# Performance work log

Measured on AMD Instinct MI355X. Metric: run time of the kernel, lower is better.

The kernel has to match this reference:

```python
import jax, jax.numpy as jnp
import numpy as np

N_CELL = 50000
N_GENE = 50000
E = 800000
D = 256
EPS = 1e-5


def setup_inputs() -> dict:
    key = jax.random.key(0)
    ks = jax.random.split(key, 12)
    inp = {
        "x_cell": jax.random.normal(ks[0], (N_CELL, D), jnp.float32),
        "x_gene": jax.random.normal(ks[1], (N_GENE, D), jnp.float32),
        "W_cg": jax.random.normal(ks[2], (D, D), jnp.float32) * (1.0 / np.sqrt(D)),
        "W_gc": jax.random.normal(ks[3], (D, D), jnp.float32) * (1.0 / np.sqrt(D)),
        "W_gg": jax.random.normal(ks[4], (D, D), jnp.float32) * (1.0 / np.sqrt(D)),
        "gamma_cell": jnp.ones((D,), jnp.float32),
        "beta_cell": jnp.zeros((D,), jnp.float32),
        "gamma_gene": jnp.ones((D,), jnp.float32),
        "beta_gene": jnp.zeros((D,), jnp.float32),
        "b_cell": jnp.zeros((D,), jnp.float32),
        "b_gene": jnp.zeros((D,), jnp.float32),
        "src_cg": jax.random.randint(ks[5], (E,), 0, N_CELL, jnp.int64 if jax.config.jax_enable_x64 else jnp.int32),
        "dst_cg": jax.random.randint(ks[6], (E,), 0, N_GENE, jnp.int64 if jax.config.jax_enable_x64 else jnp.int32),
        "src_gc": jax.random.randint(ks[7], (E,), 0, N_GENE, jnp.int64 if jax.config.jax_enable_x64 else jnp.int32),
        "dst_gc": jax.random.randint(ks[8], (E,), 0, N_CELL, jnp.int64 if jax.config.jax_enable_x64 else jnp.int32),
        "src_gg": jax.random.randint(ks[9], (E,), 0, N_GENE, jnp.int64 if jax.config.jax_enable_x64 else jnp.int32),
        "dst_gg": jax.random.randint(ks[10], (E,), 0, N_GENE, jnp.int64 if jax.config.jax_enable_x64 else jnp.int32),
    }
    return inp


def _graph_conv(x_src, src, dst, n_src, n_dst, W):
    """DGL GraphConv with norm='both': D_dst^{-1/2} A D_src^{-1/2} X W."""
    ones = jnp.ones(src.shape[0], x_src.dtype)
    deg_out = jnp.clip(jax.ops.segment_sum(ones, src, num_segments=n_src), 1.0)
    deg_in = jnp.clip(jax.ops.segment_sum(ones, dst, num_segments=n_dst), 1.0)
    h = x_src * jax.lax.rsqrt(deg_out)[:, None]          # [n_src, D]
    agg = jax.ops.segment_sum(h[src], dst, num_segments=n_dst)  # gather+scatter
    agg = agg * jax.lax.rsqrt(deg_in)[:, None]           # [n_dst, D]
    return agg @ W


def _post(h, gamma, beta, b):
    # LayerNorm (affine) -> + h_bias -> relu -> dropout(p=0, eval = identity)
    mu = jnp.mean(h, axis=-1, keepdims=True)
    var = jnp.mean((h - mu) ** 2, axis=-1, keepdims=True)
    h = (h - mu) * jax.lax.rsqrt(var + EPS) * gamma + beta
    return jax.nn.relu(h + b)


def reference(x_cell, x_gene, W_cg, W_gc, W_gg, gamma_cell, beta_cell,
              gamma_gene, beta_gene, b_cell, b_gene,
              src_cg, dst_cg, src_gc, dst_gc, src_gg, dst_gg):
    # HeteroGraphConv with aggregate='sum' across relations per dst ntype
    h_gene = (_graph_conv(x_cell, src_cg, dst_cg, N_CELL, N_GENE, W_cg)
              + _graph_conv(x_gene, src_gg, dst_gg, N_GENE, N_GENE, W_gg))
    h_cell = _graph_conv(x_gene, src_gc, dst_gc, N_GENE, N_CELL, W_gc)
    out_cell = _post(h_cell, gamma_cell, beta_cell, b_cell)
    out_gene = _post(h_gene, gamma_gene, beta_gene, b_gene)
    return jnp.stack([out_cell, out_gene])  # [2, 50000, 256]
```

## Files before the change

kernel.cpp:

```cpp
#include <hip/hip_runtime.h>
#include <hip/hip_bf16.h>
#include <stdint.h>

#define DDIM 256
#define NSHARD 8
#define T1 4096
#define NCPAD 128
#define CCAP 9216

typedef short s8v __attribute__((ext_vector_type(8)));
typedef float f4v __attribute__((ext_vector_type(4)));

__device__ __forceinline__ float bf2f(unsigned u) { return __uint_as_float(u << 16); }
__device__ __forceinline__ unsigned short f2bf(float f) {
    __hip_bfloat16 h = __float2bfloat16(f);
    return *reinterpret_cast<unsigned short*>(&h);
}
__device__ __forceinline__ unsigned pack2(float a, float b) {
    return (unsigned)f2bf(a) | ((unsigned)f2bf(b) << 16);
}

__global__ void transpose3_k(const float* __restrict__ W0, const float* __restrict__ W1,
                             const float* __restrict__ W2, __hip_bfloat16* __restrict__ T0,
                             __hip_bfloat16* __restrict__ T1v, __hip_bfloat16* __restrict__ T2) {
    const float* W = (blockIdx.y == 0) ? W0 : (blockIdx.y == 1) ? W1 : W2;
    __hip_bfloat16* T = (blockIdx.y == 0) ? T0 : (blockIdx.y == 1) ? T1v : T2;
    T[blockIdx.x * DDIM + threadIdx.x] = __float2bfloat16(W[threadIdx.x * DDIM + blockIdx.x]);
}

__global__ __launch_bounds__(256) void bin1_k(
    const int* __restrict__ s0, const int* __restrict__ d0,
    const int* __restrict__ s1, const int* __restrict__ d1,
    const int* __restrict__ s2, const int* __restrict__ d2,
    int* __restrict__ cs_shard,
    int* __restrict__ gcur,
    unsigned* __restrict__ recs,
    int N, int E) {
    __shared__ unsigned stage[T1];
    __shared__ int hcnt[NCPAD], hoff[NCPAD], lbase[NCPAD], lcur[NCPAD];
    const int t = threadIdx.x;
    const int rel = blockIdx.y;
    const int* s = (rel == 0) ? s0 : (rel == 1) ? s1 : s2;
    const int* d = (rel == 0) ? d0 : (rel == 1) ? d1 : d2;
    const int e0 = blockIdx.x * T1;
    const int n = min(T1, E - e0);
    int* csb = cs_shard + ((size_t)(blockIdx.x & (NSHARD - 1)) * 3 + rel) * N;

    if (t < NCPAD) { hcnt[t] = 0; lcur[t] = 0; }
    __syncthreads();

    int ssr[T1 / 256], ddr[T1 / 256];
    #pragma unroll
    for (int k = 0; k < T1 / 256; ++k) {
        const int li = k * 256 + t;
        const bool v = li < n;
        ssr[k] = v ? s[e0 + li] : -1;
        ddr[k] = v ? d[e0 + li] : -1;
        if (v) {
            atomicAdd(&hcnt[ddr[k] >> 9], 1);
            atomicAdd(&csb[ssr[k]], 1);
        }
    }
    __syncthreads();

    if (t < 64) {
        const int a0 = hcnt[2 * t], a1 = hcnt[2 * t + 1];
        const int sum = a0 + a1;
        int incl = sum;
        #pragma unroll
        for (int off = 1; off < 64; off <<= 1) {
            const int u = __shfl_up(incl, off);
            if (t >= off) incl += u;
        }
        const int excl = incl - sum;
        hoff[2 * t] = excl;
        hoff[2 * t + 1] = excl + a0;
    }
    __syncthreads();
    if (t < NCPAD) lbase[t] = atomicAdd(&gcur[rel * NCPAD + t], hcnt[t]);
    __syncthreads();

    #pragma unroll
    for (int k = 0; k < T1 / 256; ++k) {
        if (ddr[k] >= 0) {
            const int b = ddr[k] >> 9;
            const int p = atomicAdd(&lcur[b], 1);
            stage[hoff[b] + p] = (unsigned)ssr[k] | ((unsigned)(ddr[k] & 511) << 16)
                                 | ((unsigned)b << 25);
        }
    }
    __syncthreads();

    for (int i = t; i < n; i += 256) {
        const unsigned r = stage[i];
        const int b = (int)(r >> 25);
        const int pos = lbase[b] + (i - hoff[b]);
        if (pos < CCAP)
            recs[((size_t)rel * NCPAD + b) * CCAP + pos] = r & 0x1FFFFFFu;
    }
}

__global__ void reduce_cs_k(const int* __restrict__ cs_shard, int* __restrict__ cs, int n3) {
    const int i = blockIdx.x * blockDim.x + threadIdx.x;
    if (i >= n3) return;
    int v = 0;
    #pragma unroll
    for (int s = 0; s < NSHARD; ++s) v += cs_shard[(size_t)s * n3 + i];
    cs[i] = v;
}

__global__ __launch_bounds__(256) void sort_k(
    unsigned* __restrict__ recs, const int* __restrict__ gcur,
    int* __restrict__ row_beg, int* __restrict__ row_cnt, int N, int ncb) {
    __shared__ unsigned stage[CCAP];
    __shared__ int rc[512], ro[512], rcur[512];
    const int t = threadIdx.x;
    const int rel = blockIdx.x / ncb, bin = blockIdx.x % ncb;
    const size_t base = ((size_t)rel * NCPAD + bin) * CCAP;
    const int n = min(gcur[rel * NCPAD + bin], CCAP);

    for (int i = t; i < 512; i += 256) rc[i] = 0;
    __syncthreads();
    for (int i = t; i < n; i += 256) {
        const unsigned r = recs[base + i];
        stage[i] = r;
        atomicAdd(&rc[(r >> 16) & 511], 1);
    }
    __syncthreads();
    if (t < 64) {
        int v[8], p[8], sum = 0;
        #pragma unroll
        for (int j = 0; j < 8; ++j) { v[j] = rc[t * 8 + j]; p[j] = sum; sum += v[j]; }
        int incl = sum;
        #pragma unroll
        for (int off = 1; off < 64; off <<= 1) {
            const int u = __shfl_up(incl, off);
            if (t >= off) incl += u;
        }
        const int excl = incl - sum;
        #pragma unroll
        for (int j = 0; j < 8; ++j) { ro[t * 8 + j] = excl + p[j]; rcur[t * 8 + j] = excl + p[j]; }
    }
    __syncthreads();
    for (int i = t; i < 512; i += 256) {
        const int grow = bin * 512 + i;
        if (grow < N) {
            row_cnt[(size_t)rel * N + grow] = rc[i];
            row_beg[(size_t)rel * N + grow] = (int)(base + ro[i]);
        }
    }
    for (int i = t; i < n; i += 256) {
        const unsigned r = stage[i];
        const int pos = atomicAdd(&rcur[(r >> 16) & 511], 1);
        recs[base + pos] = r & 0xffffu;
    }
}

__global__ __launch_bounds__(256, 2) void gemm2_k(
    const float* __restrict__ X,
    const __hip_bfloat16* __restrict__ Wt0, const __hip_bfloat16* __restrict__ Wt1,
    const int* __restrict__ deg0, const int* __restrict__ deg1,
    __hip_bfloat16* __restrict__ Y0, __hip_bfloat16* __restrict__ Y1, int M) {
    const int lane = threadIdx.x & 63, wid = threadIdx.x >> 6;
    const int c = lane & 15, kb = lane >> 4;
    const int rA = blockIdx.x * 128 + wid * 32 + c;
    const int rB = rA + 16;
    const bool vA = rA < M, vB = rB < M;
    const int rAc = vA ? rA : (M - 1), rBc = vB ? rB : (M - 1);

    s8v xfA[8], xfB[8];
    const float* xA = X + (size_t)rAc * DDIM;
    const float* xB = X + (size_t)rBc * DDIM;
    #pragma unroll
    for (int ks = 0; ks < 8; ++ks) {
        const int k0 = ks * 32 + kb * 8;
        const f4v a0 = *reinterpret_cast<const f4v*>(xA + k0);
        const f4v a1 = *reinterpret_cast<const f4v*>(xA + k0 + 4);
        const f4v b0 = *reinterpret_cast<const f4v*>(xB + k0);
        const f4v b1 = *reinterpret_cast<const f4v*>(xB + k0 + 4);
        union { s8v v; unsigned short u[8]; } fa, fb;
        #pragma unroll
        for (int j = 0; j < 4; ++j) {
            fa.u[j] = f2bf(a0[j]); fa.u[4 + j] = f2bf(a1[j]);
            fb.u[j] = f2bf(b0[j]); fb.u[4 + j] = f2bf(b1[j]);
        }
        xfA[ks] = fa.v; xfB[ks] = fb.v;
    }

    const int dA0 = deg0[rAc], dB0 = deg0[rBc], dA1 = deg1[rAc], dB1 = deg1[rBc];
    const float s0A = rsqrtf((float)(dA0 < 1 ? 1 : dA0));
    const float s0B = rsqrtf((float)(dB0 < 1 ? 1 : dB0));
    const float s1A = rsqrtf((float)(dA1 < 1 ? 1 : dA1));
    const float s1B = rsqrtf((float)(dB1 < 1 ? 1 : dB1));

    #pragma unroll 2
    for (int nt = 0; nt < 16; ++nt) {
        const __hip_bfloat16* w0p = Wt0 + (size_t)(nt * 16 + c) * DDIM + kb * 8;
        const __hip_bfloat16* w1p = Wt1 + (size_t)(nt * 16 + c) * DDIM + kb * 8;
        s8v wf0[8], wf1[8];
        #pragma unroll
        for (int ks = 0; ks < 8; ++ks) {
            wf0[ks] = *reinterpret_cast<const s8v*>(w0p + ks * 32);
            wf1[ks] = *reinterpret_cast<const s8v*>(w1p + ks * 32);
        }
        f4v a00 = (f4v){0.f,0.f,0.f,0.f}, a01 = a00, a10 = a00, a11 = a00;
        #pragma unroll
        for (int ks = 0; ks < 8; ++ks) {
            a00 = __builtin_amdgcn_mfma_f32_16x16x32_bf16(wf0[ks], xfA[ks], a00, 0, 0, 0);
            a10 = __builtin_amdgcn_mfma_f32_16x16x32_bf16(wf0[ks], xfB[ks], a10, 0, 0, 0);
            a01 = __builtin_amdgcn_mfma_f32_16x16x32_bf16(wf1[ks], xfA[ks], a01, 0, 0, 0);
            a11 = __builtin_amdgcn_mfma_f32_16x16x32_bf16(wf1[ks], xfB[ks], a11, 0, 0, 0);
        }
        const int col = nt * 16 + kb * 4;
        if (vA) {
            uint2 o0, o1;
            o0.x = pack2(a00[0] * s0A, a00[1] * s0A); o0.y = pack2(a00[2] * s0A, a00[3] * s0A);
            o1.x = pack2(a01[0] * s1A, a01[1] * s1A); o1.y = pack2(a01[2] * s1A, a01[3] * s1A);
            *reinterpret_cast<uint2*>(Y0 + (size_t)rA * DDIM + col) = o0;
            *reinterpret_cast<uint2*>(Y1 + (size_t)rA * DDIM + col) = o1;
        }
        if (vB) {
            uint2 o0, o1;
            o0.x = pack2(a10[0] * s0B, a10[1] * s0B); o0.y = pack2(a10[2] * s0B, a10[3] * s0B);
            o1.x = pack2(a11[0] * s1B, a11[1] * s1B); o1.y = pack2(a11[2] * s1B, a11[3] * s1B);
            *reinterpret_cast<uint2*>(Y0 + (size_t)rB * DDIM + col) = o0;
            *reinterpret_cast<uint2*>(Y1 + (size_t)rB * DDIM + col) = o1;
        }
    }
}

__global__ __launch_bounds__(256, 2) void gemm1_k(
    const float* __restrict__ X, const __hip_bfloat16* __restrict__ Wt0,
    const int* __restrict__ deg0, __hip_bfloat16* __restrict__ Y0, int M) {
    const int lane = threadIdx.x & 63, wid = threadIdx.x >> 6;
    const int c = lane & 15, kb = lane >> 4;
    const int rA = blockIdx.x * 128 + wid * 32 + c;
    const int rB = rA + 16;
    const bool vA = rA < M, vB = rB < M;
    const int rAc = vA ? rA : (M - 1), rBc = vB ? rB : (M - 1);

    s8v xfA[8], xfB[8];
    const float* xA = X + (size_t)rAc * DDIM;
    const float* xB = X + (size_t)rBc * DDIM;
    #pragma unroll
    for (int ks = 0; ks < 8; ++ks) {
        const int k0 = ks * 32 + kb * 8;
        const f4v a0 = *reinterpret_cast<const f4v*>(xA + k0);
        const f4v a1 = *reinterpret_cast<const f4v*>(xA + k0 + 4);
        const f4v b0 = *reinterpret_cast<const f4v*>(xB + k0);
        const f4v b1 = *reinterpret_cast<const f4v*>(xB + k0 + 4);
        union { s8v v; unsigned short u[8]; } fa, fb;
        #pragma unroll
        for (int j = 0; j < 4; ++j) {
            fa.u[j] = f2bf(a0[j]); fa.u[4 + j] = f2bf(a1[j]);
            fb.u[j] = f2bf(b0[j]); fb.u[4 + j] = f2bf(b1[j]);
        }
        xfA[ks] = fa.v; xfB[ks] = fb.v;
    }
    const int dA0 = deg0[rAc], dB0 = deg0[rBc];
    const float s0A = rsqrtf((float)(dA0 < 1 ? 1 : dA0));
    const float s0B = rsqrtf((float)(dB0 < 1 ? 1 : dB0));

    #pragma unroll 2
    for (int nt = 0; nt < 16; ++nt) {
        const __hip_bfloat16* w0p = Wt0 + (size_t)(nt * 16 + c) * DDIM + kb * 8;
        s8v wf0[8];
        #pragma unroll
        for (int ks = 0; ks < 8; ++ks) wf0[ks] = *reinterpret_cast<const s8v*>(w0p + ks * 32);
        f4v a00 = (f4v){0.f,0.f,0.f,0.f}, a10 = a00;
        #pragma unroll
        for (int ks = 0; ks < 8; ++ks) {
            a00 = __builtin_amdgcn_mfma_f32_16x16x32_bf16(wf0[ks], xfA[ks], a00, 0, 0, 0);
            a10 = __builtin_amdgcn_mfma_f32_16x16x32_bf16(wf0[ks], xfB[ks], a10, 0, 0, 0);
        }
        const int col = nt * 16 + kb * 4;
        if (vA) {
            uint2 o;
            o.x = pack2(a00[0] * s0A, a00[1] * s0A); o.y = pack2(a00[2] * s0A, a00[3] * s0A);
            *reinterpret_cast<uint2*>(Y0 + (size_t)rA * DDIM + col) = o;
        }
        if (vB) {
            uint2 o;
            o.x = pack2(a10[0] * s0B, a10[1] * s0B); o.y = pack2(a10[2] * s0B, a10[3] * s0B);
            *reinterpret_cast<uint2*>(Y0 + (size_t)rB * DDIM + col) = o;
        }
    }
}

__device__ __forceinline__ void addv(f4v& a, uint2 v) {
    a[0] += bf2f(v.x & 0xffffu);
    a[1] += bf2f(v.x >> 16);
    a[2] += bf2f(v.y & 0xffffu);
    a[3] += bf2f(v.y >> 16);
}

__device__ __forceinline__ f4v segsum(const unsigned* __restrict__ recs, int beg, int n,
                                      const __hip_bfloat16* __restrict__ Y, int lane) {
    f4v a = (f4v){0.f, 0.f, 0.f, 0.f};
    for (int j0 = 0; j0 < n; j0 += 64) {
        const int chunk = min(64, n - j0);
        unsigned rv = 0;
        if (lane < chunk) rv = recs[beg + j0 + lane];
        int t = 0;
        for (; t + 8 <= chunk; t += 8) {
            uint2 v[8];
            #pragma unroll
            for (int i = 0; i < 8; ++i) {
                const int s = (int)(__shfl(rv, t + i) & 0xffffu);
                v[i] = reinterpret_cast<const uint2*>(Y + (size_t)s * DDIM)[lane];
            }
            #pragma unroll
            for (int i = 0; i < 8; ++i) addv(a, v[i]);
        }
        if (t + 4 <= chunk) {
            uint2 v[4];
            #pragma unroll
            for (int i = 0; i < 4; ++i) {
                const int s = (int)(__shfl(rv, t + i) & 0xffffu);
                v[i] = reinterpret_cast<const uint2*>(Y + (size_t)s * DDIM)[lane];
            }
            #pragma unroll
            for (int i = 0; i < 4; ++i) addv(a, v[i]);
            t += 4;
        }
        for (; t < chunk; ++t) {
            const int s = (int)(__shfl(rv, t) & 0xffffu);
            addv(a, reinterpret_cast<const uint2*>(Y + (size_t)s * DDIM)[lane]);
        }
    }
    return a;
}

__global__ __launch_bounds__(256, 4) void gather_ln_k(
    const unsigned* __restrict__ recs,
    const int* __restrict__ beg0, const int* __restrict__ cnt0,
    const __hip_bfloat16* __restrict__ Y0,
    const int* __restrict__ beg1, const int* __restrict__ cnt1,
    const __hip_bfloat16* __restrict__ Y1,
    const float* __restrict__ gamma, const float* __restrict__ beta,
    const float* __restrict__ bias, float* __restrict__ out, int n_dst) {
    const int lane = threadIdx.x & 63, wid = threadIdx.x >> 6;
    const int row = blockIdx.x * 4 + wid;
    if (row >= n_dst) return;

    const int n0 = cnt0[row];
    f4v a = segsum(recs, beg0[row], n0, Y0, lane);
    a *= rsqrtf((float)(n0 < 1 ? 1 : n0));
    if (beg1 != nullptr) {
        const int n1 = cnt1[row];
        f4v a1 = segsum(recs, beg1[row], n1, Y1, lane);
        a += a1 * rsqrtf((float)(n1 < 1 ? 1 : n1));
    }

    float s1 = a[0] + a[1] + a[2] + a[3];
    float s2 = a[0]*a[0] + a[1]*a[1] + a[2]*a[2] + a[3]*a[3];
    #pragma unroll
    for (int off = 1; off < 64; off <<= 1) {
        s1 += __shfl_xor(s1, off);
        s2 += __shfl_xor(s2, off);
    }
    const float mu = s1 * (1.f / 256.f);
    float var = s2 * (1.f / 256.f) - mu * mu;
    var = fmaxf(var, 0.f);
    const float rs = rsqrtf(var + 1e-5f);

    const f4v g  = reinterpret_cast<const f4v*>(gamma)[lane];
    const f4v be = reinterpret_cast<const f4v*>(beta)[lane];
    const f4v bb = reinterpret_cast<const f4v*>(bias)[lane];
    f4v o;
    #pragma unroll
    for (int j = 0; j < 4; ++j) {
        float v = (a[j] - mu) * rs * g[j] + be[j] + bb[j];
        o[j] = fmaxf(v, 0.f);
    }
    reinterpret_cast<f4v*>(out + (size_t)row * DDIM)[lane] = o;
}

extern "C" void kernel_launch(void* const* d_in, const int* in_sizes, int n_in,
                              void* d_out, int out_size, void* d_ws, size_t ws_size,
                              hipStream_t stream) {
    const float* x_cell     = (const float*)d_in[0];
    const float* x_gene     = (const float*)d_in[1];
    const float* W_cg       = (const float*)d_in[2];
    const float* W_gc       = (const float*)d_in[3];
    const float* W_gg       = (const float*)d_in[4];
    const float* gamma_cell = (const float*)d_in[5];
    const float* beta_cell  = (const float*)d_in[6];
    const float* gamma_gene = (const float*)d_in[7];
    const float* beta_gene  = (const float*)d_in[8];
    const float* b_cell     = (const float*)d_in[9];
    const float* b_gene     = (const float*)d_in[10];
    const int* src_cg = (const int*)d_in[11];
    const int* dst_cg = (const int*)d_in[12];
    const int* src_gc = (const int*)d_in[13];
    const int* dst_gc = (const int*)d_in[14];
    const int* src_gg = (const int*)d_in[15];
    const int* dst_gg = (const int*)d_in[16];

    const int N = in_sizes[0] / DDIM;
    const int E = in_sizes[11];
    const int ncb = (N + 511) >> 9;

    char* wsb = (char*)d_ws;
    size_t off = 0;
    __hip_bfloat16* Y_gc = (__hip_bfloat16*)(wsb + off); off += (size_t)N * DDIM * 2;
    unsigned* recs = (unsigned*)(wsb + off);             off += (size_t)3 * NCPAD * CCAP * 4;
    int* row_beg = (int*)(wsb + off);                    off += (size_t)3 * N * 4;
    int* row_cnt = (int*)(wsb + off);                    off += (size_t)3 * N * 4;
    int* cs      = (int*)(wsb + off);                    off += (size_t)3 * N * 4;
    const size_t zeroOff = off;
    int* cs_shard = (int*)(wsb + off);                   off += (size_t)NSHARD * 3 * N * 4;
    int* gcur     = (int*)(wsb + off);                   off += (size_t)3 * NCPAD * 4;
    const size_t zeroBytes = off - zeroOff;
    __hip_bfloat16* Wt_gc = (__hip_bfloat16*)(wsb + off); off += (size_t)DDIM * DDIM * 2;
    __hip_bfloat16* Wt_cg = (__hip_bfloat16*)(wsb + off); off += (size_t)DDIM * DDIM * 2;
    __hip_bfloat16* Wt_gg = (__hip_bfloat16*)(wsb + off);

    int* cs_gc = cs, *cs_cg = cs + N, *cs_gg = cs + 2 * N;
    int* beg_gc = row_beg, *beg_cg = row_beg + N, *beg_gg = row_beg + 2 * N;
    int* cnt_gc = row_cnt, *cnt_cg = row_cnt + N, *cnt_gg = row_cnt + 2 * N;

    float* out_cell = (float*)d_out;
    float* out_gene = out_cell + (size_t)N * DDIM;
    __hip_bfloat16* Y_cg = (__hip_bfloat16*)d_out;
    __hip_bfloat16* Y_gg = Y_cg + (size_t)N * DDIM;

    const int binBlocks  = (E + T1 - 1) / T1;
    const int gemmBlocks = (N + 127) / 128;
    const int gatherBlocks = (N + 3) / 4;

    transpose3_k<<<dim3(DDIM, 3), DDIM, 0, stream>>>(W_gc, W_cg, W_gg, Wt_gc, Wt_cg, Wt_gg);
    hipMemsetAsync(wsb + zeroOff, 0, zeroBytes, stream);

    bin1_k<<<dim3(binBlocks, 3), 256, 0, stream>>>(src_gc, dst_gc, src_cg, dst_cg,
                                                   src_gg, dst_gg, cs_shard, gcur, recs, N, E);
    reduce_cs_k<<<(3 * N + 255) / 256, 256, 0, stream>>>(cs_shard, cs, 3 * N);
    sort_k<<<3 * ncb, 256, 0, stream>>>(recs, gcur, row_beg, row_cnt, N, ncb);

    gemm2_k<<<gemmBlocks, 256, 0, stream>>>(x_gene, Wt_gc, Wt_gg, cs_gc, cs_gg,
                                            Y_gc, Y_gg, N);
    gemm1_k<<<gemmBlocks, 256, 0, stream>>>(x_cell, Wt_cg, cs_cg, Y_cg, N);

    gather_ln_k<<<gatherBlocks, 256, 0, stream>>>(recs, beg_cg, cnt_cg, Y_cg,
                                                  beg_gg, cnt_gg, Y_gg,
                                                  gamma_gene, beta_gene, b_gene, out_gene, N);
    gather_ln_k<<<gatherBlocks, 256, 0, stream>>>(recs, beg_gc, cnt_gc, Y_gc,
                                                  nullptr, nullptr, nullptr,
                                                  gamma_cell, beta_cell, b_cell, out_cell, N);
}
```

Baseline: 420.1 us.

## Split neighbor gather into column slices and move LayerNorm to separate pass

```diff
diff --git a/kernel.cpp b/kernel.cpp
--- a/kernel.cpp
+++ b/kernel.cpp
@@ -7,6 +7,7 @@
 #define T1 4096
 #define NCPAD 128
 #define CCAP 9216
+#define NSLICE 8
 
 typedef short s8v __attribute__((ext_vector_type(8)));
 typedef float f4v __attribute__((ext_vector_type(4)));
@@ -287,71 +288,89 @@
     }
 }
 
-__device__ __forceinline__ void addv(f4v& a, uint2 v) {
-    a[0] += bf2f(v.x & 0xffffu);
-    a[1] += bf2f(v.x >> 16);
-    a[2] += bf2f(v.y & 0xffffu);
-    a[3] += bf2f(v.y >> 16);
-}
-
-__device__ __forceinline__ f4v segsum(const unsigned* __restrict__ recs, int beg, int n,
-                                      const __hip_bfloat16* __restrict__ Y, int lane) {
-    f4v a = (f4v){0.f, 0.f, 0.f, 0.f};
+__device__ __forceinline__ void segsum_slice(const unsigned* __restrict__ recs, int beg, int n,
+                                             const __hip_bfloat16* __restrict__ Y,
+                                             int lane, int g, int scol, f4v& a0, f4v& a1) {
     for (int j0 = 0; j0 < n; j0 += 64) {
         const int chunk = min(64, n - j0);
         unsigned rv = 0;
         if (lane < chunk) rv = recs[beg + j0 + lane];
-        int t = 0;
-        for (; t + 8 <= chunk; t += 8) {
-            uint2 v[8];
-            #pragma unroll
-            for (int i = 0; i < 8; ++i) {
-                const int s = (int)(__shfl(rv, t + i) & 0xffffu);
-                v[i] = reinterpret_cast<const uint2*>(Y + (size_t)s * DDIM)[lane];
+        for (int t = 0; t < chunk; t += 16) {
+            const int e = t + g;
+            const unsigned r = __shfl(rv, e);
+            if (e < chunk) {
+                const uint4 v = *reinterpret_cast<const uint4*>(
+                    Y + (size_t)(r & 0xffffu) * DDIM + scol);
+                a0[0] += bf2f(v.x & 0xffffu); a0[1] += bf2f(v.x >> 16);
+                a0[2] += bf2f(v.y & 0xffffu); a0[3] += bf2f(v.y >> 16);
+                a1[0] += bf2f(v.z & 0xffffu); a1[1] += bf2f(v.z >> 16);
+                a1[2] += bf2f(v.w & 0xffffu); a1[3] += bf2f(v.w >> 16);
             }
-            #pragma unroll
-            for (int i = 0; i < 8; ++i) addv(a, v[i]);
-        }
-        if (t + 4 <= chunk) {
-            uint2 v[4];
-            #pragma unroll
-            for (int i = 0; i < 4; ++i) {
-                const int s = (int)(__shfl(rv, t + i) & 0xffffu);
-                v[i] = reinterpret_cast<const uint2*>(Y + (size_t)s * DDIM)[lane];
-            }
-            #pragma unroll
-            for (int i = 0; i < 4; ++i) addv(a, v[i]);
-            t += 4;
-        }
-        for (; t < chunk; ++t) {
-            const int s = (int)(__shfl(rv, t) & 0xffffu);
-            addv(a, reinterpret_cast<const uint2*>(Y + (size_t)s * DDIM)[lane]);
-        }
-    }
-    return a;
-}
-
-__global__ __launch_bounds__(256, 4) void gather_ln_k(
+        }
+    }
+}
+
+__global__ __launch_bounds__(256) void gather_slice_k(
     const unsigned* __restrict__ recs,
     const int* __restrict__ beg0, const int* __restrict__ cnt0,
     const __hip_bfloat16* __restrict__ Y0,
     const int* __restrict__ beg1, const int* __restrict__ cnt1,
     const __hip_bfloat16* __restrict__ Y1,
-    const float* __restrict__ gamma, const float* __restrict__ beta,
-    const float* __restrict__ bias, float* __restrict__ out, int n_dst) {
+    float* __restrict__ out, int n_dst) {
     const int lane = threadIdx.x & 63, wid = threadIdx.x >> 6;
     const int row = blockIdx.x * 4 + wid;
     if (row >= n_dst) return;
-
-    const int n0 = cnt0[row];
-    f4v a = segsum(recs, beg0[row], n0, Y0, lane);
-    a *= rsqrtf((float)(n0 < 1 ? 1 : n0));
+    const int g = lane >> 2;
+    const int sub = lane & 3;
+    const int scol = blockIdx.y * 32 + sub * 8;
+
+    f4v t0 = (f4v){0.f,0.f,0.f,0.f}, t1 = t0;
+    {
+        f4v a0 = t0, a1 = t0;
+        const int n0 = cnt0[row];
+        segsum_slice(recs, beg0[row], n0, Y0, lane, g, scol, a0, a1);
+        const float sc = rsqrtf((float)(n0 < 1 ? 1 : n0));
+        t0 = a0 * sc; t1 = a1 * sc;
+    }
     if (beg1 != nullptr) {
+        f4v a0 = (f4v){0.f,0.f,0.f,0.f}, a1 = a0;
         const int n1 = cnt1[row];
-        f4v a1 = segsum(recs, beg1[row], n1, Y1, lane);
-        a += a1 * rsqrtf((float)(n1 < 1 ? 1 : n1));
-    }
-
+        segsum_slice(recs, beg1[row], n1, Y1, lane, g, scol, a0, a1);
+        const float sc = rsqrtf((float)(n1 < 1 ? 1 : n1));
+        t0 += a0 * sc; t1 += a1 * sc;
+    }
+
+    #pragma unroll
+    for (int off = 4; off < 64; off <<= 1) {
+        #pragma unroll
+        for (int j = 0; j < 4; ++j) {
+            t0[j] += __shfl_xor(t0[j], off);
+            t1[j] += __shfl_xor(t1[j], off);
+        }
+    }
+    if (g == 0) {
+        float* op = out + (size_t)row * DDIM + scol;
+        *reinterpret_cast<f4v*>(op) = t0;
+        *reinterpret_cast<f4v*>(op + 4) = t1;
+    }
+}
+
+__global__ __launch_bounds__(256) void ln_k(
+    float* __restrict__ out,
+    const float* __restrict__ gamma_c, const float* __restrict__ beta_c,
+    const float* __restrict__ bias_c,
+    const float* __restrict__ gamma_g, const float* __restrict__ beta_g,
+    const float* __restrict__ bias_g, int N) {
+    const int lane = threadIdx.x & 63, wid = threadIdx.x >> 6;
+    const int row = blockIdx.x * 4 + wid;
+    if (row >= 2 * N) return;
+    const bool cell = row < N;
+    const float* gamma = cell ? gamma_c : gamma_g;
+    const float* beta  = cell ? beta_c  : beta_g;
+    const float* bias  = cell ? bias_c  : bias_g;
+
+    float* rp = out + (size_t)row * DDIM;
+    const f4v a = reinterpret_cast<const f4v*>(rp)[lane];
     float s1 = a[0] + a[1] + a[2] + a[3];
     float s2 = a[0]*a[0] + a[1]*a[1] + a[2]*a[2] + a[3]*a[3];
     #pragma unroll
@@ -369,11 +388,9 @@
     const f4v bb = reinterpret_cast<const f4v*>(bias)[lane];
     f4v o;
     #pragma unroll
-    for (int j = 0; j < 4; ++j) {
-        float v = (a[j] - mu) * rs * g[j] + be[j] + bb[j];
-        o[j] = fmaxf(v, 0.f);
-    }
-    reinterpret_cast<f4v*>(out + (size_t)row * DDIM)[lane] = o;
+    for (int j = 0; j < 4; ++j)
+        o[j] = fmaxf((a[j] - mu) * rs * g[j] + be[j] + bb[j], 0.f);
+    reinterpret_cast<f4v*>(rp)[lane] = o;
 }
 
 extern "C" void kernel_launch(void* const* d_in, const int* in_sizes, int n_in,
@@ -427,7 +444,7 @@
 
     const int binBlocks  = (E + T1 - 1) / T1;
     const int gemmBlocks = (N + 127) / 128;
-    const int gatherBlocks = (N + 3) / 4;
+    const int rowBlocks  = (N + 3) / 4;
 
     transpose3_k<<<dim3(DDIM, 3), DDIM, 0, stream>>>(W_gc, W_cg, W_gg, Wt_gc, Wt_cg, Wt_gg);
     hipMemsetAsync(wsb + zeroOff, 0, zeroBytes, stream);
@@ -441,10 +458,12 @@
                                             Y_gc, Y_gg, N);
     gemm1_k<<<gemmBlocks, 256, 0, stream>>>(x_cell, Wt_cg, cs_cg, Y_cg, N);
 
-    gather_ln_k<<<gatherBlocks, 256, 0, stream>>>(recs, beg_cg, cnt_cg, Y_cg,
-                                                  beg_gg, cnt_gg, Y_gg,
-                                                  gamma_gene, beta_gene, b_gene, out_gene, N);
-    gather_ln_k<<<gatherBlocks, 256, 0, stream>>>(recs, beg_gc, cnt_gc, Y_gc,
-                                                  nullptr, nullptr, nullptr,
-                                                  gamma_cell, beta_cell, b_cell, out_cell, N);
-}
+    gather_slice_k<<<dim3(rowBlocks, NSLICE), 256, 0, stream>>>(
+        recs, beg_cg, cnt_cg, Y_cg, beg_gg, cnt_gg, Y_gg, out_gene, N);
+    gather_slice_k<<<dim3(rowBlocks, NSLICE), 256, 0, stream>>>(
+        recs, beg_gc, cnt_gc, Y_gc, nullptr, nullptr, nullptr, out_cell, N);
+
+    ln_k<<<(2 * N + 3) / 4, 256, 0, stream>>>(out_cell,
+                                              gamma_cell, beta_cell, b_cell,
+                                              gamma_gene, beta_gene, b_gene, N);
+}
```

New measurement: 660.7 us. 57.3% more time.

## Fuse sort and GEMMs into one launch; gather two rows per wave

Applied to the files above, without the earlier changes.

```diff
diff --git a/kernel.cpp b/kernel.cpp
--- a/kernel.cpp
+++ b/kernel.cpp
@@ -100,22 +100,20 @@
     }
 }
 
-__global__ void reduce_cs_k(const int* __restrict__ cs_shard, int* __restrict__ cs, int n3) {
-    const int i = blockIdx.x * blockDim.x + threadIdx.x;
-    if (i >= n3) return;
+__device__ __forceinline__ int deg_sum(const int* __restrict__ cs_shard, int rel, int r, int N) {
     int v = 0;
     #pragma unroll
-    for (int s = 0; s < NSHARD; ++s) v += cs_shard[(size_t)s * n3 + i];
-    cs[i] = v;
-}
-
-__global__ __launch_bounds__(256) void sort_k(
-    unsigned* __restrict__ recs, const int* __restrict__ gcur,
-    int* __restrict__ row_beg, int* __restrict__ row_cnt, int N, int ncb) {
+    for (int s = 0; s < NSHARD; ++s) v += cs_shard[((size_t)s * 3 + rel) * N + r];
+    return v;
+}
+
+__device__ void sort_body(int sb, unsigned* __restrict__ recs, const int* __restrict__ gcur,
+                          int* __restrict__ row_beg, int* __restrict__ row_cnt,
+                          int N, int ncb) {
     __shared__ unsigned stage[CCAP];
     __shared__ int rc[512], ro[512], rcur[512];
     const int t = threadIdx.x;
-    const int rel = blockIdx.x / ncb, bin = blockIdx.x % ncb;
+    const int rel = sb / ncb, bin = sb % ncb;
     const size_t base = ((size_t)rel * NCPAD + bin) * CCAP;
     const int n = min(gcur[rel * NCPAD + bin], CCAP);
 
@@ -156,14 +154,15 @@
     }
 }
 
-__global__ __launch_bounds__(256, 2) void gemm2_k(
-    const float* __restrict__ X,
-    const __hip_bfloat16* __restrict__ Wt0, const __hip_bfloat16* __restrict__ Wt1,
-    const int* __restrict__ deg0, const int* __restrict__ deg1,
-    __hip_bfloat16* __restrict__ Y0, __hip_bfloat16* __restrict__ Y1, int M) {
+__device__ void gemm2_body(int gb, const float* __restrict__ X,
+                           const __hip_bfloat16* __restrict__ Wt0,
+                           const __hip_bfloat16* __restrict__ Wt1,
+                           const int* __restrict__ cs_shard, int rel0, int rel1,
+                           __hip_bfloat16* __restrict__ Y0, __hip_bfloat16* __restrict__ Y1,
+                           int M, int N) {
     const int lane = threadIdx.x & 63, wid = threadIdx.x >> 6;
     const int c = lane & 15, kb = lane >> 4;
-    const int rA = blockIdx.x * 128 + wid * 32 + c;
+    const int rA = gb * 128 + wid * 32 + c;
     const int rB = rA + 16;
     const bool vA = rA < M, vB = rB < M;
     const int rAc = vA ? rA : (M - 1), rBc = vB ? rB : (M - 1);
@@ -187,7 +186,8 @@
         xfA[ks] = fa.v; xfB[ks] = fb.v;
     }
 
-    const int dA0 = deg0[rAc], dB0 = deg0[rBc], dA1 = deg1[rAc], dB1 = deg1[rBc];
+    const int dA0 = deg_sum(cs_shard, rel0, rAc, N), dB0 = deg_sum(cs_shard, rel0, rBc, N);
+    const int dA1 = deg_sum(cs_shard, rel1, rAc, N), dB1 = deg_sum(cs_shard, rel1, rBc, N);
     const float s0A = rsqrtf((float)(dA0 < 1 ? 1 : dA0));
     const float s0B = rsqrtf((float)(dB0 < 1 ? 1 : dB0));
     const float s1A = rsqrtf((float)(dA1 < 1 ? 1 : dA1));
@@ -229,12 +229,13 @@
     }
 }
 
-__global__ __launch_bounds__(256, 2) void gemm1_k(
-    const float* __restrict__ X, const __hip_bfloat16* __restrict__ Wt0,
-    const int* __restrict__ deg0, __hip_bfloat16* __restrict__ Y0, int M) {
+__device__ void gemm1_body(int gb, const float* __restrict__ X,
+                           const __hip_bfloat16* __restrict__ Wt0,
+                           const int* __restrict__ cs_shard, int rel0,
+                           __hip_bfloat16* __restrict__ Y0, int M, int N) {
     const int lane = threadIdx.x & 63, wid = threadIdx.x >> 6;
     const int c = lane & 15, kb = lane >> 4;
-    const int rA = blockIdx.x * 128 + wid * 32 + c;
+    const int rA = gb * 128 + wid * 32 + c;
     const int rB = rA + 16;
     const bool vA = rA < M, vB = rB < M;
     const int rAc = vA ? rA : (M - 1), rBc = vB ? rB : (M - 1);
@@ -257,7 +258,7 @@
         }
         xfA[ks] = fa.v; xfB[ks] = fb.v;
     }
-    const int dA0 = deg0[rAc], dB0 = deg0[rBc];
+    const int dA0 = deg_sum(cs_shard, rel0, rAc, N), dB0 = deg_sum(cs_shard, rel0, rBc, N);
     const float s0A = rsqrtf((float)(dA0 < 1 ? 1 : dA0));
     const float s0B = rsqrtf((float)(dB0 < 1 ? 1 : dB0));
 
@@ -287,6 +288,29 @@
     }
 }
 
+__global__ __launch_bounds__(256, 2) void mid_k(
+    unsigned* __restrict__ recs, const int* __restrict__ gcur,
+    int* __restrict__ row_beg, int* __restrict__ row_cnt,
+    const float* __restrict__ x_gene, const float* __restrict__ x_cell,
+    const __hip_bfloat16* __restrict__ Wt_gc, const __hip_bfloat16* __restrict__ Wt_gg,
+    const __hip_bfloat16* __restrict__ Wt_cg,
+    const int* __restrict__ cs_shard,
+    __hip_bfloat16* __restrict__ Y_gc, __hip_bfloat16* __restrict__ Y_gg,
+    __hip_bfloat16* __restrict__ Y_cg,
+    int N, int ncb, int gemmBlocks) {
+    const int nSort = 3 * ncb;
+    const int bid = blockIdx.x;
+    if (bid < nSort) {
+        sort_body(bid, recs, gcur, row_beg, row_cnt, N, ncb);
+        return;
+    }
+    const int g = bid - nSort;
+    if (g < gemmBlocks)
+        gemm2_body(g, x_gene, Wt_gc, Wt_gg, cs_shard, 0, 2, Y_gc, Y_gg, N, N);
+    else
+        gemm1_body(g - gemmBlocks, x_cell, Wt_cg, cs_shard, 1, Y_cg, N, N);
+}
+
 __device__ __forceinline__ void addv(f4v& a, uint2 v) {
     a[0] += bf2f(v.x & 0xffffu);
     a[1] += bf2f(v.x >> 16);
@@ -294,41 +318,36 @@
     a[3] += bf2f(v.y >> 16);
 }
 
-__device__ __forceinline__ f4v segsum(const unsigned* __restrict__ recs, int beg, int n,
-                                      const __hip_bfloat16* __restrict__ Y, int lane) {
-    f4v a = (f4v){0.f, 0.f, 0.f, 0.f};
-    for (int j0 = 0; j0 < n; j0 += 64) {
-        const int chunk = min(64, n - j0);
-        unsigned rv = 0;
-        if (lane < chunk) rv = recs[beg + j0 + lane];
-        int t = 0;
-        for (; t + 8 <= chunk; t += 8) {
-            uint2 v[8];
+__device__ __forceinline__ void segsum2(const unsigned* __restrict__ recs,
+                                        int begA, int nA, int begB, int nB,
+                                        const __hip_bfloat16* __restrict__ Y,
+                                        int lane, f4v& aA, f4v& aB) {
+    const int nmax = nA > nB ? nA : nB;
+    for (int j0 = 0; j0 < nmax; j0 += 64) {
+        const int cA = nA - j0, cB = nB - j0;
+        unsigned rvA = 0, rvB = 0;
+        if (lane < cA) rvA = recs[begA + j0 + lane];
+        if (lane < cB) rvB = recs[begB + j0 + lane];
+        const int eA = cA > 64 ? 64 : cA;
+        const int eB = cB > 64 ? 64 : cB;
+        const int cm = eA > eB ? eA : eB;
+        for (int t = 0; t < cm; t += 4) {
+            uint2 vA[4], vB[4];
+            const int kA = eA - t, kB = eB - t;
             #pragma unroll
-            for (int i = 0; i < 8; ++i) {
-                const int s = (int)(__shfl(rv, t + i) & 0xffffu);
-                v[i] = reinterpret_cast<const uint2*>(Y + (size_t)s * DDIM)[lane];
-            }
+            for (int i = 0; i < 4; ++i)
+                if (i < kA) vA[i] = reinterpret_cast<const uint2*>(
+                    Y + (size_t)(__shfl(rvA, t + i) & 0xffffu) * DDIM)[lane];
             #pragma unroll
-            for (int i = 0; i < 8; ++i) addv(a, v[i]);
-        }
-        if (t + 4 <= chunk) {
-            uint2 v[4];
+            for (int i = 0; i < 4; ++i)
+                if (i < kB) vB[i] = reinterpret_cast<const uint2*>(
+                    Y + (size_t)(__shfl(rvB, t + i) & 0xffffu) * DDIM)[lane];
             #pragma unroll
-            for (int i = 0; i < 4; ++i) {
-                const int s = (int)(__shfl(rv, t + i) & 0xffffu);
-                v[i] = reinterpret_cast<const uint2*>(Y + (size_t)s * DDIM)[lane];
-            }
+            for (int i = 0; i < 4; ++i) if (i < kA) addv(aA, vA[i]);
             #pragma unroll
-            for (int i = 0; i < 4; ++i) addv(a, v[i]);
-            t += 4;
-        }
-        for (; t < chunk; ++t) {
-            const int s = (int)(__shfl(rv, t) & 0xffffu);
-            addv(a, reinterpret_cast<const uint2*>(Y + (size_t)s * DDIM)[lane]);
-        }
-    }
-    return a;
+            for (int i = 0; i < 4; ++i) if (i < kB) addv(aB, vB[i]);
+        }
+    }
 }
 
 __global__ __launch_bounds__(256, 4) void gather_ln_k(
@@ -340,40 +359,53 @@
     const float* __restrict__ gamma, const float* __restrict__ beta,
     const float* __restrict__ bias, float* __restrict__ out, int n_dst) {
     const int lane = threadIdx.x & 63, wid = threadIdx.x >> 6;
-    const int row = blockIdx.x * 4 + wid;
-    if (row >= n_dst) return;
-
-    const int n0 = cnt0[row];
-    f4v a = segsum(recs, beg0[row], n0, Y0, lane);
-    a *= rsqrtf((float)(n0 < 1 ? 1 : n0));
+    const int rA = (blockIdx.x * 4 + wid) * 2;
+    if (rA >= n_dst) return;
+    const int rB = rA + 1;
+    const bool hasB = rB < n_dst;
+    const int rBc = hasB ? rB : rA;
+
+    f4v aA = (f4v){0.f,0.f,0.f,0.f}, aB = aA;
+    const int n0A = cnt0[rA], n0B = hasB ? cnt0[rBc] : 0;
+    segsum2(recs, beg0[rA], n0A, beg0[rBc], n0B, Y0, lane, aA, aB);
+    aA *= rsqrtf((float)(n0A < 1 ? 1 : n0A));
+    aB *= rsqrtf((float)(n0B < 1 ? 1 : n0B));
     if (beg1 != nullptr) {
-        const int n1 = cnt1[row];
-        f4v a1 = segsum(recs, beg1[row], n1, Y1, lane);
-        a += a1 * rsqrtf((float)(n1 < 1 ? 1 : n1));
-    }
-
-    float s1 = a[0] + a[1] + a[2] + a[3];
-    float s2 = a[0]*a[0] + a[1]*a[1] + a[2]*a[2] + a[3]*a[3];
+        f4v bA = (f4v){0.f,0.f,0.f,0.f}, bB = bA;
+        const int n1A = cnt1[rA], n1B = hasB ? cnt1[rBc] : 0;
+        segsum2(recs, beg1[rA], n1A, beg1[rBc], n1B, Y1, lane, bA, bB);
+        aA += bA * rsqrtf((float)(n1A < 1 ? 1 : n1A));
+        aB += bB * rsqrtf((float)(n1B < 1 ? 1 : n1B));
+    }
+
+    float s1A = aA[0]+aA[1]+aA[2]+aA[3];
+    float s2A = aA[0]*aA[0]+aA[1]*aA[1]+aA[2]*aA[2]+aA[3]*aA[3];
+    float s1B = aB[0]+aB[1]+aB[2]+aB[3];
+    float s2B = aB[0]*aB[0]+aB[1]*aB[1]+aB[2]*aB[2]+aB[3]*aB[3];
     #pragma unroll
     for (int off = 1; off < 64; off <<= 1) {
-        s1 += __shfl_xor(s1, off);
-        s2 += __shfl_xor(s2, off);
-    }
-    const float mu = s1 * (1.f / 256.f);
-    float var = s2 * (1.f / 256.f) - mu * mu;
-    var = fmaxf(var, 0.f);
-    const float rs = rsqrtf(var + 1e-5f);
+        s1A += __shfl_xor(s1A, off);
+        s2A += __shfl_xor(s2A, off);
+        s1B += __shfl_xor(s1B, off);
+        s2B += __shfl_xor(s2B, off);
+    }
+    const float muA = s1A * (1.f / 256.f);
+    const float muB = s1B * (1.f / 256.f);
+    const float rsA = rsqrtf(fmaxf(s2A * (1.f / 256.f) - muA * muA, 0.f) + 1e-5f);
+    const float rsB = rsqrtf(fmaxf(s2B * (1.f / 256.f) - muB * muB, 0.f) + 1e-5f);
 
     const f4v g  = reinterpret_cast<const f4v*>(gamma)[lane];
     const f4v be = reinterpret_cast<const f4v*>(beta)[lane];
     const f4v bb = reinterpret_cast<const f4v*>(bias)[lane];
-    f4v o;
+    f4v oA, oB;
     #pragma unroll
     for (int j = 0; j < 4; ++j) {
-        float v = (a[j] - mu) * rs * g[j] + be[j] + bb[j];
-        o[j] = fmaxf(v, 0.f);
-    }
-    reinterpret_cast<f4v*>(out + (size_t)row * DDIM)[lane] = o;
+        oA[j] = fmaxf((aA[j] - muA) * rsA * g[j] + be[j] + bb[j], 0.f);
+        oB[j] = fmaxf((aB[j] - muB) * rsB * g[j] + be[j] + bb[j], 0.f);
+    }
+    reinterpret_cast<f4v*>(out + (size_t)rA * DDIM)[lane] = oA;
+    if (hasB)
+        reinterpret_cast<f4v*>(out + (size_t)rB * DDIM)[lane] = oB;
 }
 
 extern "C" void kernel_launch(void* const* d_in, const int* in_sizes, int n_in,
@@ -407,7 +439,6 @@
     unsigned* recs = (unsigned*)(wsb + off);             off += (size_t)3 * NCPAD * CCAP * 4;
     int* row_beg = (int*)(wsb + off);                    off += (size_t)3 * N * 4;
     int* row_cnt = (int*)(wsb + off);                    off += (size_t)3 * N * 4;
-    int* cs      = (int*)(wsb + off);                    off += (size_t)3 * N * 4;
     const size_t zeroOff = off;
     int* cs_shard = (int*)(wsb + off);                   off += (size_t)NSHARD * 3 * N * 4;
     int* gcur     = (int*)(wsb + off);                   off += (size_t)3 * NCPAD * 4;
@@ -416,7 +447,6 @@
     __hip_bfloat16* Wt_cg = (__hip_bfloat16*)(wsb + off); off += (size_t)DDIM * DDIM * 2;
     __hip_bfloat16* Wt_gg = (__hip_bfloat16*)(wsb + off);
 
-    int* cs_gc = cs, *cs_cg = cs + N, *cs_gg = cs + 2 * N;
     int* beg_gc = row_beg, *beg_cg = row_beg + N, *beg_gg = row_beg + 2 * N;
     int* cnt_gc = row_cnt, *cnt_cg = row_cnt + N, *cnt_gg = row_cnt + 2 * N;
 
@@ -427,19 +457,17 @@
 
     const int binBlocks  = (E + T1 - 1) / T1;
     const int gemmBlocks = (N + 127) / 128;
-    const int gatherBlocks = (N + 3) / 4;
+    const int gatherBlocks = (N + 7) / 8;
 
     transpose3_k<<<dim3(DDIM, 3), DDIM, 0, stream>>>(W_gc, W_cg, W_gg, Wt_gc, Wt_cg, Wt_gg);
     hipMemsetAsync(wsb + zeroOff, 0, zeroBytes, stream);
 
     bin1_k<<<dim3(binBlocks, 3), 256, 0, stream>>>(src_gc, dst_gc, src_cg, dst_cg,
                                                    src_gg, dst_gg, cs_shard, gcur, recs, N, E);
-    reduce_cs_k<<<(3 * N + 255) / 256, 256, 0, stream>>>(cs_shard, cs, 3 * N);
-    sort_k<<<3 * ncb, 256, 0, stream>>>(recs, gcur, row_beg, row_cnt, N, ncb);
-
-    gemm2_k<<<gemmBlocks, 256, 0, stream>>>(x_gene, Wt_gc, Wt_gg, cs_gc, cs_gg,
-                                            Y_gc, Y_gg, N);
-    gemm1_k<<<gemmBlocks, 256, 0, stream>>>(x_cell, Wt_cg, cs_cg, Y_cg, N);
+
+    mid_k<<<3 * ncb + 2 * gemmBlocks, 256, 0, stream>>>(
+        recs, gcur, row_beg, row_cnt, x_gene, x_cell,
+        Wt_gc, Wt_gg, Wt_cg, cs_shard, Y_gc, Y_gg, Y_cg, N, ncb, gemmBlocks);
 
     gather_ln_k<<<gatherBlocks, 256, 0, stream>>>(recs, beg_cg, cnt_cg, Y_cg,
                                                   beg_gg, cnt_gg, Y_gg,
```

Result: no change. 424.7 us (+1.1%).

## Stage weight tiles in double-buffered swizzled LDS for the dense GEMM kernels

Applied to the files above, without the earlier changes.

```diff
diff --git a/kernel.cpp b/kernel.cpp
--- a/kernel.cpp
+++ b/kernel.cpp
@@ -156,12 +156,14 @@
     }
 }
 
-__global__ __launch_bounds__(256, 2) void gemm2_k(
+__global__ __launch_bounds__(256, 4) void gemm2_k(
     const float* __restrict__ X,
     const __hip_bfloat16* __restrict__ Wt0, const __hip_bfloat16* __restrict__ Wt1,
     const int* __restrict__ deg0, const int* __restrict__ deg1,
     __hip_bfloat16* __restrict__ Y0, __hip_bfloat16* __restrict__ Y1, int M) {
-    const int lane = threadIdx.x & 63, wid = threadIdx.x >> 6;
+    __shared__ __hip_bfloat16 wlds[2][2][16][DDIM];
+    const int t = threadIdx.x;
+    const int lane = t & 63, wid = t >> 6;
     const int c = lane & 15, kb = lane >> 4;
     const int rA = blockIdx.x * 128 + wid * 32 + c;
     const int rB = rA + 16;
@@ -193,23 +195,43 @@
     const float s1A = rsqrtf((float)(dA1 < 1 ? 1 : dA1));
     const float s1B = rsqrtf((float)(dB1 < 1 ? 1 : dB1));
 
+    {
+        #pragma unroll
+        for (int j = 0; j < 4; ++j) {
+            const int q = t + j * 256;
+            const int rel = q >> 9, rt = (q >> 5) & 15, ch = q & 31;
+            const __hip_bfloat16* Wsrc = rel ? Wt1 : Wt0;
+            const uint4 v = *reinterpret_cast<const uint4*>(Wsrc + (size_t)rt * DDIM + ch * 8);
+            *reinterpret_cast<uint4*>(&wlds[0][rel][rt][(ch ^ (rt & 7)) * 8]) = v;
+        }
+    }
+
     #pragma unroll 2
     for (int nt = 0; nt < 16; ++nt) {
-        const __hip_bfloat16* w0p = Wt0 + (size_t)(nt * 16 + c) * DDIM + kb * 8;
-        const __hip_bfloat16* w1p = Wt1 + (size_t)(nt * 16 + c) * DDIM + kb * 8;
-        s8v wf0[8], wf1[8];
+        __syncthreads();
+        uint4 sv[4];
+        if (nt + 1 < 16) {
+            #pragma unroll
+            for (int j = 0; j < 4; ++j) {
+                const int q = t + j * 256;
+                const int rel = q >> 9, rt = (q >> 5) & 15, ch = q & 31;
+                const __hip_bfloat16* Wsrc = rel ? Wt1 : Wt0;
+                sv[j] = *reinterpret_cast<const uint4*>(
+                    Wsrc + (size_t)((nt + 1) * 16 + rt) * DDIM + ch * 8);
+            }
+        }
+
+        const int buf = nt & 1;
+        f4v a00 = (f4v){0.f,0.f,0.f,0.f}, a01 = a00, a10 = a00, a11 = a00;
         #pragma unroll
         for (int ks = 0; ks < 8; ++ks) {
-            wf0[ks] = *reinterpret_cast<const s8v*>(w0p + ks * 32);
-            wf1[ks] = *reinterpret_cast<const s8v*>(w1p + ks * 32);
-        }
-        f4v a00 = (f4v){0.f,0.f,0.f,0.f}, a01 = a00, a10 = a00, a11 = a00;
-        #pragma unroll
-        for (int ks = 0; ks < 8; ++ks) {
-            a00 = __builtin_amdgcn_mfma_f32_16x16x32_bf16(wf0[ks], xfA[ks], a00, 0, 0, 0);
-            a10 = __builtin_amdgcn_mfma_f32_16x16x32_bf16(wf0[ks], xfB[ks], a10, 0, 0, 0);
-            a01 = __builtin_amdgcn_mfma_f32_16x16x32_bf16(wf1[ks], xfA[ks], a01, 0, 0, 0);
-            a11 = __builtin_amdgcn_mfma_f32_16x16x32_bf16(wf1[ks], xfB[ks], a11, 0, 0, 0);
+            const int chs = ((kb + 4 * ks) ^ (c & 7)) * 8;
+            const s8v wf0 = *reinterpret_cast<const s8v*>(&wlds[buf][0][c][chs]);
+            const s8v wf1 = *reinterpret_cast<const s8v*>(&wlds[buf][1][c][chs]);
+            a00 = __builtin_amdgcn_mfma_f32_16x16x32_bf16(wf0, xfA[ks], a00, 0, 0, 0);
+            a10 = __builtin_amdgcn_mfma_f32_16x16x32_bf16(wf0, xfB[ks], a10, 0, 0, 0);
+            a01 = __builtin_amdgcn_mfma_f32_16x16x32_bf16(wf1, xfA[ks], a01, 0, 0, 0);
+            a11 = __builtin_amdgcn_mfma_f32_16x16x32_bf16(wf1, xfB[ks], a11, 0, 0, 0);
         }
         const int col = nt * 16 + kb * 4;
         if (vA) {
@@ -226,13 +248,24 @@
             *reinterpret_cast<uint2*>(Y0 + (size_t)rB * DDIM + col) = o0;
             *reinterpret_cast<uint2*>(Y1 + (size_t)rB * DDIM + col) = o1;
         }
-    }
-}
-
-__global__ __launch_bounds__(256, 2) void gemm1_k(
+
+        if (nt + 1 < 16) {
+            #pragma unroll
+            for (int j = 0; j < 4; ++j) {
+                const int q = t + j * 256;
+                const int rel = q >> 9, rt = (q >> 5) & 15, ch = q & 31;
+                *reinterpret_cast<uint4*>(&wlds[buf ^ 1][rel][rt][(ch ^ (rt & 7)) * 8]) = sv[j];
+            }
+        }
+    }
+}
+
+__global__ __launch_bounds__(256, 4) void gemm1_k(
     const float* __restrict__ X, const __hip_bfloat16* __restrict__ Wt0,
     const int* __restrict__ deg0, __hip_bfloat16* __restrict__ Y0, int M) {
-    const int lane = threadIdx.x & 63, wid = threadIdx.x >> 6;
+    __shared__ __hip_bfloat16 wlds[2][16][DDIM];
+    const int t = threadIdx.x;
+    const int lane = t & 63, wid = t >> 6;
     const int c = lane & 15, kb = lane >> 4;
     const int rA = blockIdx.x * 128 + wid * 32 + c;
     const int rB = rA + 16;
@@ -261,17 +294,38 @@
     const float s0A = rsqrtf((float)(dA0 < 1 ? 1 : dA0));
     const float s0B = rsqrtf((float)(dB0 < 1 ? 1 : dB0));
 
+    {
+        #pragma unroll
+        for (int j = 0; j < 2; ++j) {
+            const int q = t + j * 256;
+            const int rt = (q >> 5) & 15, ch = q & 31;
+            const uint4 v = *reinterpret_cast<const uint4*>(Wt0 + (size_t)rt * DDIM + ch * 8);
+            *reinterpret_cast<uint4*>(&wlds[0][rt][(ch ^ (rt & 7)) * 8]) = v;
+        }
+    }
+
     #pragma unroll 2
     for (int nt = 0; nt < 16; ++nt) {
-        const __hip_bfloat16* w0p = Wt0 + (size_t)(nt * 16 + c) * DDIM + kb * 8;
-        s8v wf0[8];
-        #pragma unroll
-        for (int ks = 0; ks < 8; ++ks) wf0[ks] = *reinterpret_cast<const s8v*>(w0p + ks * 32);
+        __syncthreads();
+        uint4 sv[2];
+        if (nt + 1 < 16) {
+            #pragma unroll
+            for (int j = 0; j < 2; ++j) {
+                const int q = t + j * 256;
+                const int rt = (q >> 5) & 15, ch = q & 31;
+                sv[j] = *reinterpret_cast<const uint4*>(
+                    Wt0 + (size_t)((nt + 1) * 16 + rt) * DDIM + ch * 8);
+            }
+        }
+
+        const int buf = nt & 1;
         f4v a00 = (f4v){0.f,0.f,0.f,0.f}, a10 = a00;
         #pragma unroll
         for (int ks = 0; ks < 8; ++ks) {
-            a00 = __builtin_amdgcn_mfma_f32_16x16x32_bf16(wf0[ks], xfA[ks], a00, 0, 0, 0);
-            a10 = __builtin_amdgcn_mfma_f32_16x16x32_bf16(wf0[ks], xfB[ks], a10, 0, 0, 0);
+            const int chs = ((kb + 4 * ks) ^ (c & 7)) * 8;
+            const s8v wf0 = *reinterpret_cast<const s8v*>(&wlds[buf][c][chs]);
+            a00 = __builtin_amdgcn_mfma_f32_16x16x32_bf16(wf0, xfA[ks], a00, 0, 0, 0);
+            a10 = __builtin_amdgcn_mfma_f32_16x16x32_bf16(wf0, xfB[ks], a10, 0, 0, 0);
         }
         const int col = nt * 16 + kb * 4;
         if (vA) {
@@ -283,6 +337,15 @@
             uint2 o;
             o.x = pack2(a10[0] * s0B, a10[1] * s0B); o.y = pack2(a10[2] * s0B, a10[3] * s0B);
             *reinterpret_cast<uint2*>(Y0 + (size_t)rB * DDIM + col) = o;
+        }
+
+        if (nt + 1 < 16) {
+            #pragma unroll
+            for (int j = 0; j < 2; ++j) {
+                const int q = t + j * 256;
+                const int rt = (q >> 5) & 15, ch = q & 31;
+                *reinterpret_cast<uint4*>(&wlds[buf ^ 1][rt][(ch ^ (rt & 7)) * 8]) = sv[j];
+            }
         }
     }
 }
```

Measured after the change: 404.9 us. 1.04x faster.
